# Kernel tuning notes

Hardware: AMD Instinct MI355X
Metric: run time of the kernel (lower is better)

The kernel has to match this reference:

```python
import jax, jax.numpy as jnp
import numpy as np

EPS = 1e-6

def rms_norm(x):
    # x / sqrt(mean(x^2, axis=-1) + eps)
    return x * jax.lax.rsqrt(jnp.mean(x * x, axis=-1, keepdims=True) + EPS)

def setup_inputs() -> dict:
    key = jax.random.key(0)
    k1, k2, k3 = jax.random.split(key, 3)
    T, B, D = 2048, 16, 1024
    x = jax.random.normal(k1, (T, B, D), dtype=jnp.float32)
    h0 = jax.random.normal(k2, (B, D), dtype=jnp.float32)
    # Orthogonal-ish init scaled by 0.5 (faithful to nn.init.orthogonal_ then *0.5)
    A = jax.random.normal(k3, (D, D), dtype=jnp.float32)
    Q, _ = jnp.linalg.qr(A)
    W = 0.5 * Q
    b = jnp.zeros((D,), dtype=jnp.float32)
    log_alpha = jnp.asarray(np.log(0.1), dtype=jnp.float32)
    return {"x": x, "h0": h0, "W": W, "b": b, "log_alpha": log_alpha}

def reference(x, h0, W, b, log_alpha):
    T, B, D = x.shape
    alpha = jnp.exp(log_alpha)
    # Precompute Wx for all timesteps: [T, B, D]
    Wx_all = jnp.einsum('tbd,ed->tbe', x, W) + b

    def step(h_prev, wx_t):
        h_raw = h_prev + alpha * wx_t
        h_new = rms_norm(h_raw)
        out = h_new * jax.nn.silu(h_new)
        return h_new, (h_new, out)

    _, (h_seq, output) = jax.lax.scan(step, h0, Wx_all)
    h = jnp.concatenate([h0[None], h_seq], axis=0)  # [T+1, B, D]
    return output, h
```

## Files before the change

### kernel.cpp

```cpp
#include <hip/hip_runtime.h>
#include <hip/hip_bf16.h>

#define TT 2048
#define BB 16
#define DD 1024
#define BD (BB*DD)
#define MR (TT*BB)
#define EPSV 1e-6f
#define INVD (1.0f/1024.0f)
#define CH 256
#define NCH (TT/CH)
#define RING 16

typedef __bf16 bf16x8_t __attribute__((ext_vector_type(8)));
typedef float  f32x4_t  __attribute__((ext_vector_type(4)));
typedef float  f32x2    __attribute__((ext_vector_type(2)));
typedef __attribute__((address_space(1))) void gvoid_t;
typedef __attribute__((address_space(3))) void lvoid_t;
typedef __attribute__((address_space(3))) float  lds_f;
typedef __attribute__((address_space(3))) float2 lds_f2;

union F4 { f32x4_t q; float4 v; f32x2 h[2]; float f[4]; };

static __device__ __forceinline__ f32x2 pk_mul(f32x2 a, f32x2 b) {
    f32x2 d; asm("v_pk_mul_f32 %0, %1, %2" : "=v"(d) : "v"(a), "v"(b)); return d;
}
static __device__ __forceinline__ f32x2 pk_fma(f32x2 a, f32x2 b, f32x2 c) {
    f32x2 d; asm("v_pk_fma_f32 %0, %1, %2, %3" : "=v"(d) : "v"(a), "v"(b), "v"(c)); return d;
}
static __device__ __forceinline__ f32x2 pk_add(f32x2 a, f32x2 b) {
    f32x2 d; asm("v_pk_add_f32 %0, %1, %2" : "=v"(d) : "v"(a), "v"(b)); return d;
}
static __device__ __forceinline__ float wave_red_sum(float ss) {
    asm volatile(
        "s_nop 1\n\t"
        "v_add_f32 %0, %0, %0 row_shr:1 bound_ctrl:0\n\t"
        "s_nop 1\n\t"
        "v_add_f32 %0, %0, %0 row_shr:2 bound_ctrl:0\n\t"
        "s_nop 1\n\t"
        "v_add_f32 %0, %0, %0 row_shr:4 bank_mask:0xe\n\t"
        "s_nop 1\n\t"
        "v_add_f32 %0, %0, %0 row_shr:8 bank_mask:0xc\n\t"
        "s_nop 1\n\t"
        "v_add_f32 %0, %0, %0 row_bcast:15 row_mask:0xa\n\t"
        "s_nop 1\n\t"
        "v_add_f32 %0, %0, %0 row_bcast:31 row_mask:0xc\n\t"
        "s_nop 1"
        : "+v"(ss));
    return __builtin_bit_cast(float, __builtin_amdgcn_readlane(__builtin_bit_cast(int, ss), 63));
}

static __device__ __forceinline__ unsigned short f2bf(float f) {
    __hip_bfloat16 h = __float2bfloat16(f);
    return __builtin_bit_cast(unsigned short, h);
}

__global__ void k_convert(const float* __restrict__ x, const float* __restrict__ W,
                          unsigned short* __restrict__ xb, unsigned short* __restrict__ wb) {
    const long NX4 = (long)MR * DD / 4;
    const long NW4 = (long)DD * DD / 4;
    const long stride = (long)gridDim.x * blockDim.x;
    for (long j = (long)blockIdx.x * blockDim.x + threadIdx.x; j < NX4 + NW4; j += stride) {
        const float4* src; unsigned short* dst; long o;
        if (j < NX4) { src = (const float4*)x; dst = xb; o = j; }
        else         { src = (const float4*)W; dst = wb; o = j - NX4; }
        float4 v = src[o];
        ushort4 u;
        u.x = f2bf(v.x); u.y = f2bf(v.y); u.z = f2bf(v.z); u.w = f2bf(v.w);
        *(ushort4*)(dst + o * 4) = u;
    }
}

__global__ __launch_bounds__(256, 2)
void k_gemm(const unsigned short* __restrict__ A, const unsigned short* __restrict__ Bw,
            const float* __restrict__ bias, float* __restrict__ C) {
    __shared__ char lds[16384];
    char* ldsA = lds;
    char* ldsB = lds + 8192;
    const int tid  = threadIdx.x;
    const int lane = tid & 63;
    const int wid  = tid >> 6;
    const int wm = wid >> 1, wn = wid & 1;
    const size_t arow0 = (size_t)blockIdx.y * 128;
    const int    brow0 = blockIdx.x * 128;

    f32x4_t acc[4][4] = {};

    const int off0 = tid * 16,        row0_ = off0 >> 6, colb0 = off0 & 63;
    const int off1 = 4096 + tid * 16, row1_ = off1 >> 6, colb1 = off1 & 63;

    for (int kk = 0; kk < DD / 32; ++kk) {
        const int kbase = kk * 32;
        __builtin_amdgcn_global_load_lds(
            (gvoid_t*)(A + (arow0 + row0_) * DD + kbase + (colb0 >> 1)),
            (lvoid_t*)(ldsA + off0), 16, 0, 0);
        __builtin_amdgcn_global_load_lds(
            (gvoid_t*)(A + (arow0 + row1_) * DD + kbase + (colb1 >> 1)),
            (lvoid_t*)(ldsA + off1), 16, 0, 0);
        __builtin_amdgcn_global_load_lds(
            (gvoid_t*)(Bw + (size_t)(brow0 + row0_) * DD + kbase + (colb0 >> 1)),
            (lvoid_t*)(ldsB + off0), 16, 0, 0);
        __builtin_amdgcn_global_load_lds(
            (gvoid_t*)(Bw + (size_t)(brow0 + row1_) * DD + kbase + (colb1 >> 1)),
            (lvoid_t*)(ldsB + off1), 16, 0, 0);
        __syncthreads();

        const int ml = lane & 15;
        const int kh = (lane >> 4) * 16;
        bf16x8_t av[4], bv[4];
        #pragma unroll
        for (int i = 0; i < 4; ++i) {
            av[i] = *(const bf16x8_t*)(ldsA + (wm * 64 + i * 16 + ml) * 64 + kh);
            bv[i] = *(const bf16x8_t*)(ldsB + (wn * 64 + i * 16 + ml) * 64 + kh);
        }
        #pragma unroll
        for (int i = 0; i < 4; ++i)
            #pragma unroll
            for (int j = 0; j < 4; ++j)
                acc[i][j] = __builtin_amdgcn_mfma_f32_16x16x32_bf16(av[i], bv[j], acc[i][j], 0, 0, 0);
        __syncthreads();
    }

    const int rq = (lane >> 4) * 4;
    const int cl = lane & 15;
    #pragma unroll
    for (int i = 0; i < 4; ++i) {
        #pragma unroll
        for (int j = 0; j < 4; ++j) {
            const int n = brow0 + wn * 64 + j * 16 + cl;
            const float bb = bias[n];
            #pragma unroll
            for (int q = 0; q < 4; ++q) {
                const size_t m = arow0 + wm * 64 + i * 16 + rq + q;
                C[m * DD + n] = acc[i][j][q] + bb;
            }
        }
    }
}

__global__ __launch_bounds__(256)
void k_gq(const float* __restrict__ Wx, const float* __restrict__ la,
          float2* __restrict__ gq_g) {
    const int b = blockIdx.y;
    const int wid = threadIdx.x >> 6, lane = threadIdx.x & 63;
    const int j0 = blockIdx.x * 16 + wid * 4;
    const float alpha = expf(la[0]);
    const float a2 = alpha * alpha;
    const int dof = lane * 4;
    const float* base = Wx + b * DD + dof;

    F4 R[5][4];
    #pragma unroll
    for (int jj = 0; jj < 5; ++jj) {
        const int row = max(j0 - 1 + jj, 0);
        #pragma unroll
        for (int k = 0; k < 4; ++k)
            R[jj][k].v = *(const float4*)(base + (size_t)row * BD + k * 256);
    }
    float red[8];
    #pragma unroll
    for (int sI = 0; sI < 4; ++sI) {
        float g = 0.f, q = 0.f;
        #pragma unroll
        for (int k = 0; k < 4; ++k)
            #pragma unroll
            for (int j = 0; j < 4; ++j) {
                const float w0 = R[sI][k].f[j], w1 = R[sI + 1][k].f[j];
                g = fmaf(w0, w1, g);
                q = fmaf(w1, w1, q);
            }
        red[sI] = g; red[4 + sI] = q;
    }
    #pragma unroll
    for (int m = 1; m < 64; m <<= 1)
        #pragma unroll
        for (int k = 0; k < 8; ++k)
            red[k] += __shfl_xor(red[k], m, 64);
    if (lane == 0) {
        #pragma unroll
        for (int sI = 0; sI < 4; ++sI) {
            const int j = j0 + sI;
            gq_g[(size_t)b * TT + j] =
                make_float2(j == 0 ? 0.f : a2 * red[sI], a2 * red[4 + sI]);
        }
    }
}

__global__ __launch_bounds__(64, 1)
void k_phaseA(const float* __restrict__ Wx, const float* __restrict__ h0,
              const float* __restrict__ la, const float2* __restrict__ gq_g,
              float* __restrict__ hout, float* __restrict__ rtab) {
    __shared__ float  ring[RING * DD];
    __shared__ float2 gqlds[TT];
    const int b = blockIdx.x;
    const int lane = threadIdx.x;
    const int dof = lane * 4;
    const float alpha = expf(la[0]);
    const float* wbase = Wx + b * DD;

    {
        const float4* src = (const float4*)(gq_g + (size_t)b * TT);
        float4* dst = (float4*)gqlds;
        #pragma unroll
        for (int i = 0; i < 16; ++i) dst[i * 64 + lane] = src[i * 64 + lane];
    }
    f32x2 hraw[8];
    #pragma unroll
    for (int k = 0; k < 4; ++k) {
        F4 u; u.v = *(const float4*)(h0 + b * DD + k * 256 + dof);
        hraw[2*k] = u.h[0]; hraw[2*k+1] = u.h[1];
        *(float4*)(hout + b * DD + k * 256 + dof) = u.v;
    }
    asm volatile("" :: "v"(hraw[0]), "v"(hraw[1]), "v"(hraw[2]), "v"(hraw[3]),
                       "v"(hraw[4]), "v"(hraw[5]), "v"(hraw[6]), "v"(hraw[7]));
    __builtin_amdgcn_sched_barrier(0);

    #pragma unroll
    for (int s = 0; s < RING; ++s)
        #pragma unroll
        for (int k = 0; k < 4; ++k)
            __builtin_amdgcn_global_load_lds(
                (gvoid_t*)(wbase + (size_t)s * BD + k * 256 + dof),
                (lvoid_t*)(ring + s * DD + k * 256), 16, 0, 0);

    asm volatile("s_waitcnt vmcnt(48)" ::: "memory");
    __builtin_amdgcn_sched_barrier(0);

    F4 wR[4][4];
    #pragma unroll
    for (int j = 0; j < 4; ++j)
        #pragma unroll
        for (int k = 0; k < 4; ++k)
            asm volatile("ds_read_b128 %0, %1"
                         : "=v"(wR[j][k].q)
                         : "v"((lds_f*)(ring + j * DD + k * 256 + dof)));
    f32x2 g2[2];
    asm volatile("ds_read_b64 %0, %1" : "=v"(g2[1]) : "v"((lds_f2*)&gqlds[0]));
    asm volatile("ds_read_b64 %0, %1" : "=v"(g2[0]) : "v"((lds_f2*)&gqlds[1]));
    asm volatile("s_waitcnt lgkmcnt(0)" ::: "memory");
    __builtin_amdgcn_sched_barrier(0);

    float ss, ee[2], vr1 = 1.f, vr2 = 1.f;
    {
        f32x2 sa = pk_mul(hraw[0], hraw[0]);
        #pragma unroll
        for (int p = 1; p < 8; ++p) sa = pk_fma(hraw[p], hraw[p], sa);
        ss = wave_red_sum(sa[0] + sa[1]);
        f32x2 da = pk_mul(hraw[0], wR[0][0].h[0]);
        f32x2 ea = pk_mul(hraw[0], wR[1][0].h[0]);
        #pragma unroll
        for (int p = 1; p < 8; ++p) {
            da = pk_fma(hraw[p], wR[0][p>>1].h[p&1], da);
            ea = pk_fma(hraw[p], wR[1][p>>1].h[p&1], ea);
        }
        ee[1] = alpha * wave_red_sum(da[0] + da[1]);
        ee[0] = alpha * wave_red_sum(ea[0] + ea[1]);
    }
    float r_keep = 0.f;

    for (int tt = 0; tt < TT; tt += RING) {
        #pragma unroll
        for (int s = 0; s < RING; ++s) {
            const int m = tt + s;
            const int pe = (s + 1) & 1;

            asm volatile("s_waitcnt lgkmcnt(5)" ::: "memory");
            __builtin_amdgcn_sched_barrier(0);

            const float Dp = fmaf(vr2, ee[pe], g2[pe][0]);
            const float u1 = fmaf(vr1, ss, Dp + Dp);
            ss = fmaf(vr1, u1, g2[pe][1]);
            const float rt = __builtin_amdgcn_rsqf(fmaf(ss, INVD, EPSV));
            r_keep = (lane == (m & 63)) ? rt : r_keep;

            const f32x2 rr1 = {vr1, vr1};
            const f32x2 aav = {alpha, alpha};
            #pragma unroll
            for (int k = 0; k < 4; ++k) {
                hraw[2*k]   = pk_fma(rr1, hraw[2*k],   pk_mul(aav, wR[s & 3][k].h[0]));
                hraw[2*k+1] = pk_fma(rr1, hraw[2*k+1], pk_mul(aav, wR[s & 3][k].h[1]));
            }

            {
                const F4* B = wR[(s + 2) & 3];
                f32x2 ea0 = pk_mul(hraw[0], B[0].h[0]);
                f32x2 ea1 = pk_mul(hraw[1], B[0].h[1]);
                f32x2 ea2 = pk_mul(hraw[2], B[1].h[0]);
                f32x2 ea3 = pk_mul(hraw[3], B[1].h[1]);
                ea0 = pk_fma(hraw[4], B[2].h[0], ea0);
                ea1 = pk_fma(hraw[5], B[2].h[1], ea1);
                ea2 = pk_fma(hraw[6], B[3].h[0], ea2);
                ea3 = pk_fma(hraw[7], B[3].h[1], ea3);
                ea0 = pk_add(ea0, ea1); ea2 = pk_add(ea2, ea3); ea0 = pk_add(ea0, ea2);
                ee[pe] = alpha * wave_red_sum(ea0[0] + ea0[1]);
            }

            {
                const float* wp = wbase + (size_t)((m + RING) & (TT - 1)) * BD;
                #pragma unroll
                for (int k = 0; k < 4; ++k)
                    __builtin_amdgcn_global_load_lds(
                        (gvoid_t*)(wp + k * 256 + dof),
                        (lvoid_t*)(ring + s * DD + k * 256), 16, 0, 0);
            }

            asm volatile("s_waitcnt vmcnt(48)" ::: "memory");
            __builtin_amdgcn_sched_barrier(0);

            #pragma unroll
            for (int k = 0; k < 4; ++k)
                asm volatile("ds_read_b128 %0, %1"
                             : "=v"(wR[s & 3][k].q)
                             : "v"((lds_f*)(ring + ((s + 4) & 15) * DD + k * 256 + dof)));
            asm volatile("ds_read_b64 %0, %1"
                         : "=v"(g2[pe]) : "v"((lds_f2*)&gqlds[(m + 2) & (TT - 1)]));

            vr2 = vr1; vr1 = rt;
        }

        if ((tt & 63) == 48)
            rtab[(size_t)b * TT + (tt - 48) + lane] = r_keep;
        if ((tt & 255) == 240) {
            float* hp = hout + (size_t)(tt + RING) * BD + b * DD;
            const f32x2 rr0 = {vr1, vr1};
            #pragma unroll
            for (int k = 0; k < 4; ++k) {
                F4 u;
                u.h[0] = pk_mul(rr0, hraw[2*k]);
                u.h[1] = pk_mul(rr0, hraw[2*k+1]);
                *(float4*)(hp + k * 256 + dof) = u.v;
            }
        }
    }

    asm volatile("s_waitcnt vmcnt(0) lgkmcnt(0)" ::: "memory");
}

__global__ __launch_bounds__(256)
void k_phaseB(float* __restrict__ WxOut, float* __restrict__ hout,
              const float* __restrict__ rtab, const float* __restrict__ la) {
    const int col = blockIdx.x * 256 + threadIdx.x;
    const int c = blockIdx.y;
    const int b = col >> 10;
    const float alpha = expf(la[0]);
    const float* rr = rtab + b * TT;
    float h = hout[(size_t)(c * CH) * BD + col];
    const int t0 = c * CH + 1;
    float w = WxOut[(size_t)(t0 - 1) * BD + col];
    for (int s = 0; s < CH; ++s) {
        const int t = t0 + s;
        float wnext = 0.f;
        if (s + 1 < CH) wnext = WxOut[(size_t)t * BD + col];
        const float r = rr[t - 1];
        const float hraw = fmaf(alpha, w, h);
        const float hn = r * hraw;
        const float sg = 1.0f / (1.0f + __expf(-hn));
        WxOut[(size_t)(t - 1) * BD + col] = hn * hn * sg;
        if ((t & (CH - 1)) != 0 || t == TT)
            hout[(size_t)t * BD + col] = hn;
        h = hn;
        w = wnext;
    }
}

extern "C" void kernel_launch(void* const* d_in, const int* in_sizes, int n_in,
                              void* d_out, int out_size, void* d_ws, size_t ws_size,
                              hipStream_t stream) {
    (void)in_sizes; (void)n_in; (void)out_size; (void)ws_size;
    const float* x    = (const float*)d_in[0];
    const float* h0   = (const float*)d_in[1];
    const float* W    = (const float*)d_in[2];
    const float* bias = (const float*)d_in[3];
    const float* la   = (const float*)d_in[4];

    float* outr = (float*)d_out;
    float* hreg = outr + (size_t)TT * BD;
    unsigned short* xb = (unsigned short*)hreg;
    unsigned short* wb = xb + (size_t)MR * DD;
    float2* gq_g = (float2*)(hreg + BD);
    float*  rtab = (float*)d_ws;

    k_convert<<<2048, 256, 0, stream>>>(x, W, xb, wb);
    k_gemm<<<dim3(DD / 128, MR / 128), 256, 0, stream>>>(xb, wb, bias, outr);
    k_gq<<<dim3(TT / 16, BB), 256, 0, stream>>>(outr, la, gq_g);
    k_phaseA<<<BB, 64, 0, stream>>>(outr, h0, la, gq_g, hreg, rtab);
    k_phaseB<<<dim3(BD / 256, NCH), 256, 0, stream>>>(outr, hreg, rtab, la);
}
```

Before: 579.3 us.

## Prefetch Wx rows directly into registers instead of staging through an LDS ring

```diff
diff --git a/kernel.cpp b/kernel.cpp
--- a/kernel.cpp
+++ b/kernel.cpp
@@ -10,14 +10,13 @@
 #define INVD (1.0f/1024.0f)
 #define CH 256
 #define NCH (TT/CH)
-#define RING 16
+#define RING 8
 
 typedef __bf16 bf16x8_t __attribute__((ext_vector_type(8)));
 typedef float  f32x4_t  __attribute__((ext_vector_type(4)));
 typedef float  f32x2    __attribute__((ext_vector_type(2)));
 typedef __attribute__((address_space(1))) void gvoid_t;
 typedef __attribute__((address_space(3))) void lvoid_t;
-typedef __attribute__((address_space(3))) float  lds_f;
 typedef __attribute__((address_space(3))) float2 lds_f2;
 
 union F4 { f32x4_t q; float4 v; f32x2 h[2]; float f[4]; };
@@ -190,13 +189,12 @@
 void k_phaseA(const float* __restrict__ Wx, const float* __restrict__ h0,
               const float* __restrict__ la, const float2* __restrict__ gq_g,
               float* __restrict__ hout, float* __restrict__ rtab) {
-    __shared__ float  ring[RING * DD];
     __shared__ float2 gqlds[TT];
     const int b = blockIdx.x;
     const int lane = threadIdx.x;
     const int dof = lane * 4;
     const float alpha = expf(la[0]);
-    const float* wbase = Wx + b * DD;
+    const float* wbase = Wx + b * DD + dof;
 
     {
         const float4* src = (const float4*)(gq_g + (size_t)b * TT);
@@ -213,31 +211,19 @@
     }
     asm volatile("" :: "v"(hraw[0]), "v"(hraw[1]), "v"(hraw[2]), "v"(hraw[3]),
                        "v"(hraw[4]), "v"(hraw[5]), "v"(hraw[6]), "v"(hraw[7]));
+    asm volatile("s_waitcnt lgkmcnt(0)" ::: "memory");
     __builtin_amdgcn_sched_barrier(0);
 
-    #pragma unroll
-    for (int s = 0; s < RING; ++s)
+    F4 buf[RING][4];
+    #pragma unroll
+    for (int s = 0; s < RING; ++s) {
+        const float* wp = wbase + (size_t)s * BD;
         #pragma unroll
         for (int k = 0; k < 4; ++k)
-            __builtin_amdgcn_global_load_lds(
-                (gvoid_t*)(wbase + (size_t)s * BD + k * 256 + dof),
-                (lvoid_t*)(ring + s * DD + k * 256), 16, 0, 0);
-
-    asm volatile("s_waitcnt vmcnt(48)" ::: "memory");
-    __builtin_amdgcn_sched_barrier(0);
-
-    F4 wR[4][4];
-    #pragma unroll
-    for (int j = 0; j < 4; ++j)
-        #pragma unroll
-        for (int k = 0; k < 4; ++k)
-            asm volatile("ds_read_b128 %0, %1"
-                         : "=v"(wR[j][k].q)
-                         : "v"((lds_f*)(ring + j * DD + k * 256 + dof)));
-    f32x2 g2[2];
-    asm volatile("ds_read_b64 %0, %1" : "=v"(g2[1]) : "v"((lds_f2*)&gqlds[0]));
-    asm volatile("ds_read_b64 %0, %1" : "=v"(g2[0]) : "v"((lds_f2*)&gqlds[1]));
-    asm volatile("s_waitcnt lgkmcnt(0)" ::: "memory");
+            asm volatile("global_load_dwordx4 %0, %1, off"
+                         : "=v"(buf[s][k].q) : "v"(wp + k * 256));
+    }
+    asm volatile("s_waitcnt vmcnt(24)" ::: "memory");
     __builtin_amdgcn_sched_barrier(0);
 
     float ss, ee[2], vr1 = 1.f, vr2 = 1.f;
@@ -246,16 +232,22 @@
         #pragma unroll
         for (int p = 1; p < 8; ++p) sa = pk_fma(hraw[p], hraw[p], sa);
         ss = wave_red_sum(sa[0] + sa[1]);
-        f32x2 da = pk_mul(hraw[0], wR[0][0].h[0]);
-        f32x2 ea = pk_mul(hraw[0], wR[1][0].h[0]);
+        f32x2 da = pk_mul(hraw[0], buf[0][0].h[0]);
+        f32x2 ea = pk_mul(hraw[0], buf[1][0].h[0]);
         #pragma unroll
         for (int p = 1; p < 8; ++p) {
-            da = pk_fma(hraw[p], wR[0][p>>1].h[p&1], da);
-            ea = pk_fma(hraw[p], wR[1][p>>1].h[p&1], ea);
+            da = pk_fma(hraw[p], buf[0][p>>1].h[p&1], da);
+            ea = pk_fma(hraw[p], buf[1][p>>1].h[p&1], ea);
         }
         ee[1] = alpha * wave_red_sum(da[0] + da[1]);
         ee[0] = alpha * wave_red_sum(ea[0] + ea[1]);
     }
+    f32x2 g2v[2];
+    asm volatile("ds_read_b64 %0, %1" : "=v"(g2v[1]) : "v"((lds_f2*)&gqlds[0]));
+    asm volatile("ds_read_b64 %0, %1" : "=v"(g2v[0]) : "v"((lds_f2*)&gqlds[1]));
+    asm volatile("s_waitcnt lgkmcnt(0)" ::: "memory");
+    __builtin_amdgcn_sched_barrier(0);
+
     float r_keep = 0.f;
 
     for (int tt = 0; tt < TT; tt += RING) {
@@ -264,12 +256,26 @@
             const int m = tt + s;
             const int pe = (s + 1) & 1;
 
-            asm volatile("s_waitcnt lgkmcnt(5)" ::: "memory");
+            if (s == 0 && (tt & 255) == 0) {
+                float* hp = hout + (size_t)tt * BD + b * DD;
+                const f32x2 rr0 = {vr1, vr1};
+                #pragma unroll
+                for (int k = 0; k < 4; ++k) {
+                    F4 u;
+                    u.h[0] = pk_mul(rr0, hraw[2*k]);
+                    u.h[1] = pk_mul(rr0, hraw[2*k+1]);
+                    *(float4*)(hp + k * 256 + dof) = u.v;
+                }
+            }
+
+            asm volatile("s_waitcnt vmcnt(20)" ::: "memory");
             __builtin_amdgcn_sched_barrier(0);
-
-            const float Dp = fmaf(vr2, ee[pe], g2[pe][0]);
+            asm volatile("s_waitcnt lgkmcnt(1)" ::: "memory");
+            __builtin_amdgcn_sched_barrier(0);
+
+            const float Dp = fmaf(vr2, ee[pe], g2v[pe][0]);
             const float u1 = fmaf(vr1, ss, Dp + Dp);
-            ss = fmaf(vr1, u1, g2[pe][1]);
+            ss = fmaf(vr1, u1, g2v[pe][1]);
             const float rt = __builtin_amdgcn_rsqf(fmaf(ss, INVD, EPSV));
             r_keep = (lane == (m & 63)) ? rt : r_keep;
 
@@ -277,12 +283,12 @@
             const f32x2 aav = {alpha, alpha};
             #pragma unroll
             for (int k = 0; k < 4; ++k) {
-                hraw[2*k]   = pk_fma(rr1, hraw[2*k],   pk_mul(aav, wR[s & 3][k].h[0]));
-                hraw[2*k+1] = pk_fma(rr1, hraw[2*k+1], pk_mul(aav, wR[s & 3][k].h[1]));
+                hraw[2*k]   = pk_fma(rr1, hraw[2*k],   pk_mul(aav, buf[s][k].h[0]));
+                hraw[2*k+1] = pk_fma(rr1, hraw[2*k+1], pk_mul(aav, buf[s][k].h[1]));
             }
 
             {
-                const F4* B = wR[(s + 2) & 3];
+                const F4* B = buf[(s + 2) & (RING - 1)];
                 f32x2 ea0 = pk_mul(hraw[0], B[0].h[0]);
                 f32x2 ea1 = pk_mul(hraw[1], B[0].h[1]);
                 f32x2 ea2 = pk_mul(hraw[2], B[1].h[0]);
@@ -295,42 +301,22 @@
                 ee[pe] = alpha * wave_red_sum(ea0[0] + ea0[1]);
             }
 
+            asm volatile("ds_read_b64 %0, %1"
+                         : "=v"(g2v[pe]) : "v"((lds_f2*)&gqlds[(m + 2) & (TT - 1)]));
+
             {
                 const float* wp = wbase + (size_t)((m + RING) & (TT - 1)) * BD;
                 #pragma unroll
                 for (int k = 0; k < 4; ++k)
-                    __builtin_amdgcn_global_load_lds(
-                        (gvoid_t*)(wp + k * 256 + dof),
-                        (lvoid_t*)(ring + s * DD + k * 256), 16, 0, 0);
-            }
-
-            asm volatile("s_waitcnt vmcnt(48)" ::: "memory");
-            __builtin_amdgcn_sched_barrier(0);
-
-            #pragma unroll
-            for (int k = 0; k < 4; ++k)
-                asm volatile("ds_read_b128 %0, %1"
-                             : "=v"(wR[s & 3][k].q)
-                             : "v"((lds_f*)(ring + ((s + 4) & 15) * DD + k * 256 + dof)));
-            asm volatile("ds_read_b64 %0, %1"
-                         : "=v"(g2[pe]) : "v"((lds_f2*)&gqlds[(m + 2) & (TT - 1)]));
+                    asm volatile("global_load_dwordx4 %0, %1, off"
+                                 : "=v"(buf[s][k].q) : "v"(wp + k * 256));
+            }
 
             vr2 = vr1; vr1 = rt;
         }
 
-        if ((tt & 63) == 48)
-            rtab[(size_t)b * TT + (tt - 48) + lane] = r_keep;
-        if ((tt & 255) == 240) {
-            float* hp = hout + (size_t)(tt + RING) * BD + b * DD;
-            const f32x2 rr0 = {vr1, vr1};
-            #pragma unroll
-            for (int k = 0; k < 4; ++k) {
-                F4 u;
-                u.h[0] = pk_mul(rr0, hraw[2*k]);
-                u.h[1] = pk_mul(rr0, hraw[2*k+1]);
-                *(float4*)(hp + k * 256 + dof) = u.v;
-            }
-        }
+        if ((tt & 63) == 56)
+            rtab[(size_t)b * TT + (tt - 56) + lane] = r_keep;
     }
 
     asm volatile("s_waitcnt vmcnt(0) lgkmcnt(0)" ::: "memory");
```

Result: faster. 542.5 us (-6.4%).
